# Kernel tuning notes

Measured on AMD Instinct MI355X. Metric: run time of the kernel, lower is better.

## Reference

```python
import jax, jax.numpy as jnp
import numpy as np

B, N, DIM, H = 4, 2048, 64, 8
SCALE = DIM ** -0.5  # qk_scale defaults to head_dim**-0.5 with head_dim = dim


def setup_inputs() -> dict:
    key = jax.random.key(0)
    k1, k2, k3 = jax.random.split(key, 3)
    x = jax.random.normal(k1, (B, N, DIM), dtype=jnp.float32)
    Wqkv = jax.random.normal(k2, (DIM, 3 * H * DIM), dtype=jnp.float32) * (DIM ** -0.5)
    Wproj = jax.random.normal(k3, (H * DIM, DIM), dtype=jnp.float32) * ((H * DIM) ** -0.5)
    bproj = jnp.zeros((DIM,), dtype=jnp.float32)
    return {"x": x, "Wqkv": Wqkv, "Wproj": Wproj, "bproj": bproj}


def reference(x, Wqkv, Wproj, bproj):
    Bx, Nx, C = x.shape
    # qkv: [B,N,3*H*C] -> [B,N,3,H,C] -> (3,B,H,N,C)
    qkv = (x @ Wqkv).reshape(Bx, Nx, 3, H, C).transpose(2, 0, 3, 1, 4)
    q, k, v = qkv[0], qkv[1], qkv[2]
    # scores: [B,H,N,N]
    attn = jax.nn.softmax(jnp.einsum('bhnc,bhmc->bhnm', q, k) * SCALE, axis=-1)
    out = jnp.einsum('bhnm,bhmc->bhnc', attn, v)  # [B,H,N,C]
    out = out.transpose(0, 2, 1, 3).reshape(Bx, Nx, H * C)  # [B,N,H*C]
    return out @ Wproj + bproj  # [B,N,C]
```

## Files before the change

### kernel.cpp

```cpp
#include <hip/hip_runtime.h>

#define NB 4
#define SEQ 2048
#define CD 64
#define NHEAD 8
#define BHN (NB * NHEAD)
#define ROWS (NB * SEQ)
#define HC 512

#define QSCALE 0.18033688011112042f
#define SHIFT  23.083120654223414f

typedef float f32x4 __attribute__((ext_vector_type(4)));
typedef short s16x8 __attribute__((ext_vector_type(8)));
typedef unsigned short u16;
typedef unsigned int u32;

__device__ __forceinline__ u16 f2bf(float x) {
  union { float f; unsigned u; } v; v.f = x;
  unsigned r = v.u + 0x7FFFu + ((v.u >> 16) & 1u);
  return (u16)(r >> 16);
}

__device__ __forceinline__ float fast_exp2(float x) {
#if __has_builtin(__builtin_amdgcn_exp2f)
  return __builtin_amdgcn_exp2f(x);
#else
  return exp2f(x);
#endif
}

__device__ __forceinline__ u32 bitsf(float x) {
  union { float f; u32 u; } v; v.f = x; return v.u;
}

__device__ __forceinline__ u32 pack_trunc(float a, float b) {
#if __has_builtin(__builtin_amdgcn_perm)
  return __builtin_amdgcn_perm(bitsf(b), bitsf(a), 0x07060302u);
#else
  return (bitsf(a) >> 16) | (bitsf(b) & 0xFFFF0000u);
#endif
}

__device__ __forceinline__ u32 pack_rne(float a, float b) {
  return (u32)f2bf(a) | ((u32)f2bf(b) << 16);
}

__device__ __forceinline__ f32x4 mfma_bf16(s16x8 a, s16x8 b, f32x4 c) {
  return __builtin_amdgcn_mfma_f32_16x16x32_bf16(a, b, c, 0, 0, 0);
}


__global__ void __launch_bounds__(256) qkv_kernel(
    const float* __restrict__ x, const float* __restrict__ Wqkv,
    const float* __restrict__ Wproj, u16* __restrict__ Q, u16* __restrict__ Kf,
    u16* __restrict__ Vf, u16* __restrict__ WpF) {
  const int t = threadIdx.x;

  if (blockIdx.x == 128) {
    for (int i = blockIdx.y * 256 + t; i < 64 * 512; i += 2048) {
      const int f = i >> 9, ln = (i >> 3) & 63, j = i & 7;
      const int col = (f & 3) * 16 + (ln & 15);
      const int k = (f >> 2) * 32 + (ln >> 4) * 8 + j;
      WpF[i] = f2bf(Wproj[k * 64 + col]);
    }
    return;
  }

  __shared__ __align__(16) u16 xs[64 * 72];
  __shared__ __align__(16) u16 wts[192 * 72];

  const int w = t >> 6, lane = t & 63, quad = lane >> 4, c16 = lane & 15;
  const int rb = blockIdx.x * 64;
  const int c0 = blockIdx.y * 192;

  {
    const int row = t >> 2, cc0 = (t & 3) * 16;
    const float* xp = x + (size_t)(rb + row) * CD + cc0;
    union { u16 u[16]; int4 v[2]; } bx;
#pragma unroll
    for (int j = 0; j < 16; j += 4) {
      float4 xv = *(const float4*)(xp + j);
      bx.u[j] = f2bf(xv.x); bx.u[j + 1] = f2bf(xv.y);
      bx.u[j + 2] = f2bf(xv.z); bx.u[j + 3] = f2bf(xv.w);
    }
    *(int4*)&xs[row * 72 + cc0] = bx.v[0];
    *(int4*)&xs[row * 72 + cc0 + 8] = bx.v[1];
  }
#pragma unroll
  for (int p = 0; p < 12; ++p) {
    const int idx = p * 256 + t;
    const int n = idx % 192, k4 = (idx / 192) * 4;
    const float* wp = Wqkv + (size_t)k4 * 1536 + c0 + n;
    const float w0 = wp[0], w1 = wp[1536], w2 = wp[3072], w3 = wp[4608];
    uint2 pk;
    pk.x = pack_rne(w0, w1);
    pk.y = pack_rne(w2, w3);
    *(uint2*)&wts[n * 72 + k4] = pk;
  }
  __syncthreads();

  s16x8 af[2];
#pragma unroll
  for (int kc = 0; kc < 2; ++kc)
    af[kc] = *(const s16x8*)&xs[(w * 16 + c16) * 72 + kc * 32 + quad * 8];

  const int rw = rb + w * 16;
  const int b = rw >> 11;
  const int nn0 = rw & (SEQ - 1);

#pragma unroll
  for (int nb = 0; nb < 12; ++nb) {
    const int cb = c0 + nb * 16;
    const int three = cb >> 9;
    const int h = (cb >> 6) & 7;
    const int ccb = cb & 63;
    const int bhv = b * NHEAD + h;
    s16x8 bf_[2];
#pragma unroll
    for (int kc = 0; kc < 2; ++kc)
      bf_[kc] = *(const s16x8*)&wts[(nb * 16 + c16) * 72 + kc * 32 + quad * 8];

    if (three == 2) {
      f32x4 acc = (f32x4){0.f, 0.f, 0.f, 0.f};
#pragma unroll
      for (int kc = 0; kc < 2; ++kc) acc = mfma_bf16(af[kc], bf_[kc], acc);
      uint2 pk;
      pk.x = pack_rne(acc[0], acc[1]);
      pk.y = pack_rne(acc[2], acc[3]);
      const int tile = nn0 >> 5;
      const int cb_ = ccb >> 4;
      const int kq = (nn0 & 31) + quad * 4;
      const size_t off = (size_t)bhv * (SEQ * CD) + (size_t)tile * 2048 +
                         cb_ * 512 + (kq >> 3) * 128 + c16 * 8 + (kq & 4);
      *(uint2*)(Vf + off) = pk;
    } else if (three == 1) {
      f32x4 acc = (f32x4){0.f, 0.f, 0.f, 0.f};
#pragma unroll
      for (int kc = 0; kc < 2; ++kc) acc = mfma_bf16(bf_[kc], af[kc], acc);
      uint2 pk;
      pk.x = pack_rne(acc[0], acc[1]);
      pk.y = pack_rne(acc[2], acc[3]);
      const int tile = nn0 >> 5;
      const int kb_ = (nn0 >> 4) & 1;
      const int cc_ = ccb >> 5;
      const int cq = (ccb & 31) + quad * 4;
      const size_t off = (size_t)bhv * (SEQ * CD) + (size_t)tile * 2048 +
                         (kb_ * 2 + cc_) * 512 + (cq >> 3) * 128 + c16 * 8 +
                         (cq & 4);
      *(uint2*)(Kf + off) = pk;
    } else {
      f32x4 acc = (f32x4){0.f, 0.f, 0.f, 0.f};
#pragma unroll
      for (int kc = 0; kc < 2; ++kc) acc = mfma_bf16(bf_[kc], af[kc], acc);
      uint2 pk;
      pk.x = pack_rne(acc[0] * QSCALE, acc[1] * QSCALE);
      pk.y = pack_rne(acc[2] * QSCALE, acc[3] * QSCALE);
      *(uint2*)(Q + ((size_t)bhv * SEQ + nn0 + c16) * CD + ccb + quad * 4) = pk;
    }
  }
}

__global__ void __launch_bounds__(128, 2) attn_kernel(
    const u16* __restrict__ Q, const u16* __restrict__ Kf,
    const u16* __restrict__ Vf, u16* __restrict__ O) {
  __shared__ __align__(16) u16 smem[8320];

  const int t = threadIdx.x;
  const int w = t >> 6, lane = t & 63, quad = lane >> 4, c16 = lane & 15;
  const int bh = blockIdx.y;
  const int q0 = blockIdx.x * 64;

  u16* Pw = smem + w * 2560;

  const u16* Qb = Q + (size_t)bh * SEQ * CD;
  const u16* KbT = Kf + (size_t)bh * (SEQ * CD) + (size_t)w * 32 * 2048 +
                   lane * 8;
  const u16* VbT = Vf + (size_t)bh * (SEQ * CD) + (size_t)w * 32 * 2048 +
                   lane * 8;

  s16x8 qfb[4][2];
#pragma unroll
  for (int qb = 0; qb < 4; ++qb)
#pragma unroll
    for (int cc = 0; cc < 2; ++cc)
      qfb[qb][cc] = *(const s16x8*)(Qb + (size_t)(q0 + qb * 16 + c16) * CD +
                                    cc * 32 + quad * 8);

  s16x8 onesf;
  {
    const short one = (c16 == 0) ? (short)0x3F80 : (short)0;
#pragma unroll
    for (int j = 0; j < 8; ++j) onesf[j] = one;
  }

  f32x4 o[4][4], osum[4];
#pragma unroll
  for (int qb = 0; qb < 4; ++qb) {
    osum[qb] = (f32x4){0.f, 0.f, 0.f, 0.f};
#pragma unroll
    for (int cb = 0; cb < 4; ++cb) o[qb][cb] = (f32x4){0.f, 0.f, 0.f, 0.f};
  }

  s16x8 ka[4], va[4], kb2[4], vb2[4];

#define LOAD_TILE(kf_, vf_, it_)                                               \
  {                                                                            \
    _Pragma("unroll") for (int fi = 0; fi < 4; ++fi)                           \
        kf_[fi] = *(const s16x8*)(KbT + (it_) * 2048 + fi * 512);              \
    _Pragma("unroll") for (int cb = 0; cb < 4; ++cb)                           \
        vf_[cb] = *(const s16x8*)(VbT + (it_) * 2048 + cb * 512);              \
  }

#define COMPUTE_TILE(kf_, vf_)                                                 \
  {                                                                            \
    _Pragma("unroll") for (int qb = 0; qb < 4; ++qb) {                         \
      u16* Pq = Pw + qb * 640;                                                 \
      _Pragma("unroll") for (int kb = 0; kb < 2; ++kb) {                       \
        f32x4 s = (f32x4){-SHIFT, -SHIFT, -SHIFT, -SHIFT};                     \
        s = mfma_bf16(kf_[kb * 2], qfb[qb][0], s);                             \
        s = mfma_bf16(kf_[kb * 2 + 1], qfb[qb][1], s);                         \
        uint2 pk;                                                              \
        pk.x = pack_trunc(fast_exp2(s[0]), fast_exp2(s[1]));                   \
        pk.y = pack_trunc(fast_exp2(s[2]), fast_exp2(s[3]));                   \
        *(uint2*)&Pq[c16 * 40 + kb * 16 + quad * 4] = pk;                      \
      }                                                                        \
      const s16x8 pf = *(const s16x8*)&Pq[c16 * 40 + quad * 8];                \
      _Pragma("unroll") for (int cb = 0; cb < 4; ++cb)                         \
          o[qb][cb] = mfma_bf16(pf, vf_[cb], o[qb][cb]);                       \
      osum[qb] = mfma_bf16(pf, onesf, osum[qb]);                               \
    }                                                                          \
  }

  LOAD_TILE(ka, va, 0)
  for (int it = 0; it < 32; it += 2) {
    if (it + 1 < 32) LOAD_TILE(kb2, vb2, it + 1)
    COMPUTE_TILE(ka, va)
    if (it + 2 < 32) LOAD_TILE(ka, va, it + 2)
    if (it + 1 < 32) COMPUTE_TILE(kb2, vb2)
  }
#undef LOAD_TILE
#undef COMPUTE_TILE

  float* X  = (float*)smem;
  float* Lx = (float*)(smem + 8192);

  __syncthreads();
  if (w == 1) {
#pragma unroll
    for (int qb = 0; qb < 4; ++qb) {
#pragma unroll
      for (int cb = 0; cb < 4; ++cb)
#pragma unroll
        for (int i = 0; i < 4; ++i)
          X[(qb * 16 + quad * 4 + i) * 64 + cb * 16 + c16] = o[qb][cb][i];
      if (c16 == 0)
#pragma unroll
        for (int i = 0; i < 4; ++i)
          Lx[qb * 16 + quad * 4 + i] = osum[qb][i];
    }
  }
  __syncthreads();
  if (w == 0) {
    const int b = bh >> 3, h = bh & 7;
#pragma unroll
    for (int qb = 0; qb < 4; ++qb) {
#pragma unroll
      for (int i = 0; i < 4; ++i) {
        const float l0 = __shfl(osum[qb][i], lane & 48);
        const int qq = qb * 16 + quad * 4 + i;
        const float inv = 1.0f / (l0 + Lx[qq]);
        const int q = q0 + qq;
        u16* dst = O + ((size_t)(b * SEQ + q)) * HC + h * CD;
#pragma unroll
        for (int cb = 0; cb < 4; ++cb)
          dst[cb * 16 + c16] =
              f2bf((o[qb][cb][i] + X[qq * 64 + cb * 16 + c16]) * inv);
      }
    }
  }
}

__global__ void __launch_bounds__(256) proj_kernel(
    const u16* __restrict__ O, const u16* __restrict__ WpF,
    const float* __restrict__ bias, float* __restrict__ out) {
  __shared__ __align__(16) u16 Ls[16 * 520];
  __shared__ __align__(16) float Cred[4][64][20];
  const int t = threadIdx.x;
  const int w = t >> 6, lane = t & 63, quad = lane >> 4, c16 = lane & 15;
  const int r0 = blockIdx.x * 16;

  s16x8 wf[4][4];
#pragma unroll
  for (int kc = 0; kc < 4; ++kc)
#pragma unroll
    for (int nb = 0; nb < 4; ++nb)
      wf[kc][nb] = *(const s16x8*)(WpF + ((((w * 4 + kc) * 4 + nb) << 9) +
                                          lane * 8));

  {
    const int row = t >> 4, cg = (t & 15) * 8;
#pragma unroll
    for (int p = 0; p < 4; ++p)
      *(int4*)&Ls[row * 520 + p * 128 + cg] =
          *(const int4*)(O + (size_t)(r0 + row) * HC + p * 128 + cg);
  }
  __syncthreads();

  f32x4 acc[4];
#pragma unroll
  for (int nb = 0; nb < 4; ++nb) acc[nb] = (f32x4){0.f, 0.f, 0.f, 0.f};
#pragma unroll
  for (int kc = 0; kc < 4; ++kc) {
    const s16x8 af =
        *(const s16x8*)&Ls[c16 * 520 + w * 128 + kc * 32 + quad * 8];
#pragma unroll
    for (int nb = 0; nb < 4; ++nb)
      acc[nb] = mfma_bf16(af, wf[kc][nb], acc[nb]);
  }

#pragma unroll
  for (int nb = 0; nb < 4; ++nb)
    *(f32x4*)&Cred[w][nb * 16 + c16][quad * 4] = acc[nb];
  __syncthreads();

  const int col = t & 63, rbase = (t >> 6) * 4;
  const float bv = bias[col];
#pragma unroll
  for (int j = 0; j < 4; ++j) {
    const int r = rbase + j;
    out[(size_t)(r0 + r) * CD + col] = Cred[0][col][r] + Cred[1][col][r] +
                                       Cred[2][col][r] + Cred[3][col][r] + bv;
  }
}

extern "C" void kernel_launch(void* const* d_in, const int* in_sizes, int n_in,
                              void* d_out, int out_size, void* d_ws, size_t ws_size,
                              hipStream_t stream) {
  (void)in_sizes; (void)n_in; (void)out_size; (void)ws_size;
  const float* x     = (const float*)d_in[0];
  const float* Wqkv  = (const float*)d_in[1];
  const float* Wproj = (const float*)d_in[2];
  const float* bproj = (const float*)d_in[3];
  float* out = (float*)d_out;

  u16* WpF = (u16*)d_ws;
  u16* Qw  = WpF + CD * HC;
  u16* Kfw = Qw + (size_t)BHN * SEQ * CD;
  u16* Vfw = Kfw + (size_t)BHN * SEQ * CD;
  u16* Ow  = Vfw + (size_t)BHN * SEQ * CD;

  qkv_kernel<<<dim3(129, 8), 256, 0, stream>>>(x, Wqkv, Wproj, Qw, Kfw, Vfw,
                                               WpF);
  attn_kernel<<<dim3(32, 32), 128, 0, stream>>>(Qw, Kfw, Vfw, Ow);
  proj_kernel<<<512, 256, 0, stream>>>(Ow, WpF, bproj, out);
}
```

Baseline: 120.8 us.

## Split attention KV range across four waves and vectorize output stores

The attention block grows from two to four wavefronts. Each wave handles a quarter of the key/value sequence (16 tiles instead of 32), and the partial outputs and row sums are combined through shared memory in four serialized phases. The final normalization is spread across all waves, and each lane writes 16 bf16 values with vector stores instead of scattered scalar stores. This gives more parallelism per query tile, at the cost of extra shared-memory reduction passes, more barriers and higher per-block resource use.

Result: slower. 456.0 us (+277.6%).

```diff
diff --git a/kernel.cpp b/kernel.cpp
--- a/kernel.cpp
+++ b/kernel.cpp
@@ -161,10 +161,10 @@
   }
 }
 
-__global__ void __launch_bounds__(128, 2) attn_kernel(
+__global__ void __launch_bounds__(256, 4) attn_kernel(
     const u16* __restrict__ Q, const u16* __restrict__ Kf,
     const u16* __restrict__ Vf, u16* __restrict__ O) {
-  __shared__ __align__(16) u16 smem[8320];
+  __shared__ __align__(16) u16 smem[10240];
 
   const int t = threadIdx.x;
   const int w = t >> 6, lane = t & 63, quad = lane >> 4, c16 = lane & 15;
@@ -174,9 +174,9 @@
   u16* Pw = smem + w * 2560;
 
   const u16* Qb = Q + (size_t)bh * SEQ * CD;
-  const u16* KbT = Kf + (size_t)bh * (SEQ * CD) + (size_t)w * 32 * 2048 +
+  const u16* KbT = Kf + (size_t)bh * (SEQ * CD) + (size_t)w * 16 * 2048 +
                    lane * 8;
-  const u16* VbT = Vf + (size_t)bh * (SEQ * CD) + (size_t)w * 32 * 2048 +
+  const u16* VbT = Vf + (size_t)bh * (SEQ * CD) + (size_t)w * 16 * 2048 +
                    lane * 8;
 
   s16x8 qfb[4][2];
@@ -233,51 +233,56 @@
   }
 
   LOAD_TILE(ka, va, 0)
-  for (int it = 0; it < 32; it += 2) {
-    if (it + 1 < 32) LOAD_TILE(kb2, vb2, it + 1)
+  for (int it = 0; it < 16; it += 2) {
+    if (it + 1 < 16) LOAD_TILE(kb2, vb2, it + 1)
     COMPUTE_TILE(ka, va)
-    if (it + 2 < 32) LOAD_TILE(ka, va, it + 2)
-    if (it + 1 < 32) COMPUTE_TILE(kb2, vb2)
+    if (it + 2 < 16) LOAD_TILE(ka, va, it + 2)
+    if (it + 1 < 16) COMPUTE_TILE(kb2, vb2)
   }
 #undef LOAD_TILE
 #undef COMPUTE_TILE
 
   float* X  = (float*)smem;
-  float* Lx = (float*)(smem + 8192);
+  float* Lx = (float*)smem + 64 * 65;
 
   __syncthreads();
-  if (w == 1) {
-#pragma unroll
-    for (int qb = 0; qb < 4; ++qb) {
-#pragma unroll
-      for (int cb = 0; cb < 4; ++cb)
-#pragma unroll
-        for (int i = 0; i < 4; ++i)
-          X[(qb * 16 + quad * 4 + i) * 64 + cb * 16 + c16] = o[qb][cb][i];
-      if (c16 == 0)
-#pragma unroll
-        for (int i = 0; i < 4; ++i)
-          Lx[qb * 16 + quad * 4 + i] = osum[qb][i];
-    }
-  }
-  __syncthreads();
-  if (w == 0) {
-    const int b = bh >> 3, h = bh & 7;
-#pragma unroll
-    for (int qb = 0; qb < 4; ++qb) {
-#pragma unroll
-      for (int i = 0; i < 4; ++i) {
-        const float l0 = __shfl(osum[qb][i], lane & 48);
-        const int qq = qb * 16 + quad * 4 + i;
-        const float inv = 1.0f / (l0 + Lx[qq]);
-        const int q = q0 + qq;
-        u16* dst = O + ((size_t)(b * SEQ + q)) * HC + h * CD;
-#pragma unroll
-        for (int cb = 0; cb < 4; ++cb)
-          dst[cb * 16 + c16] =
-              f2bf((o[qb][cb][i] + X[qq * 64 + cb * 16 + c16]) * inv);
+#pragma unroll
+  for (int ph = 0; ph < 4; ++ph) {
+    if (w == ph) {
+#pragma unroll
+      for (int qb = 0; qb < 4; ++qb) {
+#pragma unroll
+        for (int i = 0; i < 4; ++i) {
+          const int qq = qb * 16 + quad * 4 + i;
+#pragma unroll
+          for (int cb = 0; cb < 4; ++cb) {
+            float* p = &X[qq * 65 + cb * 16 + c16];
+            if (ph == 0) *p = o[qb][cb][i];
+            else *p += o[qb][cb][i];
+          }
+          if (c16 == 0) {
+            float* p = &Lx[qq];
+            if (ph == 0) *p = osum[qb][i];
+            else *p += osum[qb][i];
+          }
+        }
       }
     }
+    __syncthreads();
+  }
+
+  {
+    const int b = bh >> 3, h = bh & 7;
+    const int r = w * 16 + (lane >> 2);
+    const int cb4 = (lane & 3) * 16;
+    const float inv = 1.0f / Lx[r];
+    union { u16 u[16]; int4 v[2]; } buf;
+#pragma unroll
+    for (int j = 0; j < 16; ++j)
+      buf.u[j] = f2bf(X[r * 65 + cb4 + j] * inv);
+    u16* dst = O + ((size_t)(b * SEQ + q0 + r)) * HC + h * CD + cb4;
+    *(int4*)dst = buf.v[0];
+    *(int4*)(dst + 8) = buf.v[1];
   }
 }
 
@@ -352,6 +357,6 @@
 
   qkv_kernel<<<dim3(129, 8), 256, 0, stream>>>(x, Wqkv, Wproj, Qw, Kfw, Vfw,
                                                WpF);
-  attn_kernel<<<dim3(32, 32), 128, 0, stream>>>(Qw, Kfw, Vfw, Ow);
+  attn_kernel<<<dim3(32, 32), 256, 0, stream>>>(Qw, Kfw, Vfw, Ow);
   proj_kernel<<<512, 256, 0, stream>>>(Ow, WpF, bproj, out);
 }
```
